# Kernel optimization log

Measured on AMD Instinct MI355X. Metric: run time of the kernel, lower is better.

## Reference

```python
import jax, jax.numpy as jnp
import numpy as np

B, S, E, FFN, Q = 8, 2048, 512, 2048, 8


def setup_inputs() -> dict:
    key = jax.random.key(0)
    k0, k1, k2, k3 = jax.random.split(key, 4)
    x = jax.random.normal(k0, (B, S, E), dtype=jnp.float32)
    ry = jax.random.normal(k1, (Q,), dtype=jnp.float32)  # trainable RY angles
    w1 = jax.random.normal(k2, (FFN, Q), dtype=jnp.float32) / np.sqrt(Q).astype(np.float32)
    b1 = jnp.zeros((FFN,), dtype=jnp.float32)
    w2 = jax.random.normal(k3, (E, FFN), dtype=jnp.float32) / np.sqrt(FFN).astype(np.float32)
    b2 = jnp.zeros((E,), dtype=jnp.float32)
    return {"x": x, "ry": ry, "w1": w1, "b1": b1, "w2": w2, "b2": b2}


def reference(x, ry, w1, b1, w2, b2):
    # Quantum layer: each qubit i starts in |0>, gets RX(x[..., i]) then RY(ry[i]),
    # then PauliZ expectation. Product state => closed form <Z_i> = cos(x_i) * cos(ry_i).
    nq = ry.shape[0]
    z = jnp.cos(x[..., :nq]) * jnp.cos(ry)  # [B, S, Q]
    # dropout is identity in eval mode
    h = jnp.einsum("bsq,fq->bsf", z, w1) + b1  # fc1
    return jnp.einsum("bsf,ef->bse", jax.nn.relu(h), w2) + b2  # fc2
```

## Files before the change

### kernel.cpp

```cpp
#include <hip/hip_runtime.h>
#include <cstdint>
#include <cstddef>


typedef __attribute__((ext_vector_type(8))) short s16x8;
typedef __attribute__((ext_vector_type(4))) float f32x4;

__device__ __forceinline__ unsigned short f2bf(float f) {
  unsigned int u = __float_as_uint(f);
  unsigned int r = u + 0x7fffu + ((u >> 16) & 1u);
  return (unsigned short)(r >> 16);
}

__device__ __forceinline__ void async_copy16(const void* g, void* l) {
  __builtin_amdgcn_global_load_lds(
      (const __attribute__((address_space(1))) void*)(uintptr_t)g,
      (__attribute__((address_space(3))) void*)(unsigned int)(uintptr_t)l,
      16, 0, 0);
}

__global__ __launch_bounds__(256) void k_w2(const float* __restrict__ w2,
                                            unsigned short* __restrict__ img) {
  const int n = blockIdx.x;
  const int t = threadIdx.x;
  const int s = t >> 2, quad = t & 3;
  const float* src = w2 + (size_t)n * 2048 + t * 8;
  float4 a = *(const float4*)src;
  float4 b = *(const float4*)(src + 4);
  uint4 pk;
  pk.x = f2bf(a.x) | ((unsigned)f2bf(a.y) << 16);
  pk.y = f2bf(a.z) | ((unsigned)f2bf(a.w) << 16);
  pk.z = f2bf(b.x) | ((unsigned)f2bf(b.y) << 16);
  pk.w = f2bf(b.z) | ((unsigned)f2bf(b.w) << 16);
  const int nt = n >> 8, nl = n & 255, nhi = nl >> 4, nlo = nl & 15;
  const size_t ci = (size_t)(nt * 64 + s) * 1024 + nhi * 64 + quad * 16 + nlo;
  *(uint4*)(img + ci * 8) = pk;
}

__global__ __launch_bounds__(256, 2) void k_fused(
    const float* __restrict__ x, const float* __restrict__ ry,
    const float* __restrict__ w1, const float* __restrict__ b1,
    const unsigned short* __restrict__ w2b, const float* __restrict__ b2,
    float* __restrict__ C) {
  __shared__ unsigned short As[2][64 * 32];
  __shared__ unsigned short Bs[2][256 * 32];
  __shared__ float b1s[2048];

  const int t = threadIdx.x;
  const int lane = t & 63;
  const int w = t >> 6;
  const int mt = (int)(blockIdx.x >> 1);
  const int nt = (int)(blockIdx.x & 1);
  const int r0 = mt * 64;
  const int c0 = nt * 256;
  const int fp = t & 15;
  const int rq = t >> 4;

  float zr[4][8];
  {
    float4 ra = *(const float4*)ry;
    float4 rb = *(const float4*)(ry + 4);
    float cy[8] = {__cosf(ra.x), __cosf(ra.y), __cosf(ra.z), __cosf(ra.w),
                   __cosf(rb.x), __cosf(rb.y), __cosf(rb.z), __cosf(rb.w)};
#pragma unroll
    for (int r = 0; r < 4; ++r) {
      const float* xr = x + (size_t)(r0 + rq * 4 + r) * 512;
      float4 x0 = *(const float4*)xr;
      float4 x1 = *(const float4*)(xr + 4);
      zr[r][0] = __cosf(x0.x) * cy[0];
      zr[r][1] = __cosf(x0.y) * cy[1];
      zr[r][2] = __cosf(x0.z) * cy[2];
      zr[r][3] = __cosf(x0.w) * cy[3];
      zr[r][4] = __cosf(x1.x) * cy[4];
      zr[r][5] = __cosf(x1.y) * cy[5];
      zr[r][6] = __cosf(x1.z) * cy[6];
      zr[r][7] = __cosf(x1.w) * cy[7];
    }
  }
  __builtin_amdgcn_sched_barrier(0);

  f32x4 wA0, wA1, wA2, wA3, wB0, wB1, wB2, wB3;
  {
    const f32x4* p0 = (const f32x4*)(w1 + fp * 16);
    wA0 = p0[0]; wA1 = p0[1]; wA2 = p0[2]; wA3 = p0[3];
    const f32x4* p1 = (const f32x4*)(w1 + 256 + fp * 16);
    wB0 = p1[0]; wB1 = p1[1]; wB2 = p1[2]; wB3 = p1[3];
  }
  __builtin_amdgcn_sched_barrier(0);

  const unsigned short* gB = w2b + (size_t)nt * 524288 + t * 8;
  char* lB = (char*)Bs + t * 16;
  auto stage = [&](int s, int buf) {
#pragma unroll
    for (int p = 0; p < 4; ++p)
      async_copy16(gB + (size_t)s * 8192 + p * 2048,
                   lB + buf * 16384 + p * 4096);
  };
  stage(0, 0);
  async_copy16(b1 + (size_t)t * 4, (char*)b1s + (size_t)t * 16);
  async_copy16(b1 + (size_t)(t + 256) * 4, (char*)b1s + (size_t)(t + 256) * 16);
  stage(1, 1);

  asm volatile("s_waitcnt vmcnt(4) lgkmcnt(0)" ::: "memory");
  __builtin_amdgcn_sched_barrier(0);
  __builtin_amdgcn_s_barrier();

  char* aswr = (char*)As + (rq >> 2) * 1024 +
               (((((fp >> 3) & 1) << 3) | ((rq & 3) << 1) | ((fp >> 2) & 1)) << 4) +
               (fp & 3) * 4;
  auto act = [&](int s, int buf, const f32x4& v0, const f32x4& v1,
                 const f32x4& v2, const f32x4& v3) {
    float b0 = b1s[s * 32 + fp * 2];
    float b1v = b1s[s * 32 + fp * 2 + 1];
    char* dst = aswr + buf * 4096;
#pragma unroll
    for (int r = 0; r < 4; ++r) {
      float h0 = b0, h1 = b1v;
      h0 += zr[r][0] * v0[0]; h1 += zr[r][0] * v2[0];
      h0 += zr[r][1] * v0[1]; h1 += zr[r][1] * v2[1];
      h0 += zr[r][2] * v0[2]; h1 += zr[r][2] * v2[2];
      h0 += zr[r][3] * v0[3]; h1 += zr[r][3] * v2[3];
      h0 += zr[r][4] * v1[0]; h1 += zr[r][4] * v3[0];
      h0 += zr[r][5] * v1[1]; h1 += zr[r][5] * v3[1];
      h0 += zr[r][6] * v1[2]; h1 += zr[r][6] * v3[2];
      h0 += zr[r][7] * v1[3]; h1 += zr[r][7] * v3[3];
      h0 = fmaxf(h0, 0.0f);
      h1 = fmaxf(h1, 0.0f);
      unsigned int u;
      asm("v_cvt_pk_bf16_f32 %0, %1, %2" : "=v"(u) : "v"(h0), "v"(h1));
      *(unsigned int*)(dst + r * 256) = u;
    }
  };

  act(0, 0, wA0, wA1, wA2, wA3);

  const int wn = w * 64;
  const int fr = lane & 15;
  const int quad = lane >> 4;
  const int slotA = ((fr & 3) << 4) | (((quad >> 1) & 1) << 3) |
                    ((fr >> 2) << 1) | (quad & 1);
  const char* pAb = (const char*)As + slotA * 16;
  const char* pBb = (const char*)Bs + w * 4096 + quad * 256 + fr * 16;

  f32x4 acc[4][4];
#pragma unroll
  for (int i = 0; i < 4; ++i)
#pragma unroll
    for (int j = 0; j < 4; ++j) acc[i][j] = (f32x4){0.f, 0.f, 0.f, 0.f};

  auto body = [&](int kt, const f32x4& u0, const f32x4& u1, const f32x4& u2,
                  const f32x4& u3, f32x4& l0, f32x4& l1, f32x4& l2,
                  f32x4& l3) {
    asm volatile("s_waitcnt vmcnt(4) lgkmcnt(0)" ::: "memory");
    __builtin_amdgcn_sched_barrier(0);
    __builtin_amdgcn_s_barrier();

    {
      const f32x4* p = (const f32x4*)(w1 + (size_t)(kt + 2) * 256 + fp * 16);
      l0 = p[0]; l1 = p[1]; l2 = p[2]; l3 = p[3];
    }
    const int cur = kt & 1;
    s16x8 af[4], bfv[4];
    const char* pA = pAb + cur * 4096;
    const char* pB = pBb + cur * 16384;
#pragma unroll
    for (int i = 0; i < 4; ++i) af[i] = *(const s16x8*)(pA + i * 1024);
#pragma unroll
    for (int j = 0; j < 4; ++j) bfv[j] = *(const s16x8*)(pB + j * 1024);

    act(kt + 1, cur ^ 1, u0, u1, u2, u3);

    __builtin_amdgcn_s_setprio(1);
#pragma unroll
    for (int i = 0; i < 4; ++i)
#pragma unroll
      for (int j = 0; j < 4; ++j)
        acc[i][j] = __builtin_amdgcn_mfma_f32_16x16x32_bf16(af[i], bfv[j],
                                                            acc[i][j], 0, 0, 0);
    __builtin_amdgcn_s_setprio(0);

    asm volatile("s_waitcnt lgkmcnt(0)" ::: "memory");
    __builtin_amdgcn_sched_barrier(0);
    __builtin_amdgcn_s_barrier();

    stage(kt + 2, cur);
  };

  for (int kt = 0; kt < 62; kt += 2) {
    body(kt, wB0, wB1, wB2, wB3, wA0, wA1, wA2, wA3);
    body(kt + 1, wA0, wA1, wA2, wA3, wB0, wB1, wB2, wB3);
  }

  {
    asm volatile("s_waitcnt vmcnt(4) lgkmcnt(0)" ::: "memory");
    __builtin_amdgcn_sched_barrier(0);
    __builtin_amdgcn_s_barrier();
    s16x8 af[4], bfv[4];
#pragma unroll
    for (int i = 0; i < 4; ++i) af[i] = *(const s16x8*)(pAb + i * 1024);
#pragma unroll
    for (int j = 0; j < 4; ++j) bfv[j] = *(const s16x8*)(pBb + j * 1024);
    act(63, 1, wB0, wB1, wB2, wB3);
    __builtin_amdgcn_s_setprio(1);
#pragma unroll
    for (int i = 0; i < 4; ++i)
#pragma unroll
      for (int j = 0; j < 4; ++j)
        acc[i][j] = __builtin_amdgcn_mfma_f32_16x16x32_bf16(af[i], bfv[j],
                                                            acc[i][j], 0, 0, 0);
    __builtin_amdgcn_s_setprio(0);
    asm volatile("s_waitcnt lgkmcnt(0)" ::: "memory");
    __builtin_amdgcn_sched_barrier(0);
    __builtin_amdgcn_s_barrier();
  }
  {
    asm volatile("s_waitcnt vmcnt(0) lgkmcnt(0)" ::: "memory");
    __builtin_amdgcn_sched_barrier(0);
    __builtin_amdgcn_s_barrier();
    s16x8 af[4], bfv[4];
#pragma unroll
    for (int i = 0; i < 4; ++i)
      af[i] = *(const s16x8*)(pAb + 4096 + i * 1024);
#pragma unroll
    for (int j = 0; j < 4; ++j)
      bfv[j] = *(const s16x8*)(pBb + 16384 + j * 1024);
#pragma unroll
    for (int i = 0; i < 4; ++i)
#pragma unroll
      for (int j = 0; j < 4; ++j)
        acc[i][j] = __builtin_amdgcn_mfma_f32_16x16x32_bf16(af[i], bfv[j],
                                                            acc[i][j], 0, 0, 0);
  }

  float bias[4];
#pragma unroll
  for (int j = 0; j < 4; ++j) bias[j] = b2[c0 + wn + j * 16 + fr];
#pragma unroll
  for (int i = 0; i < 4; ++i) {
    const int rbase = r0 + i * 16 + quad * 4;
#pragma unroll
    for (int rr = 0; rr < 4; ++rr) {
      float* crow = C + (size_t)(rbase + rr) * 512;
#pragma unroll
      for (int j = 0; j < 4; ++j)
        crow[c0 + wn + j * 16 + fr] = acc[i][j][rr] + bias[j];
    }
  }
}

__global__ __launch_bounds__(256) void k_naive(
    const float* __restrict__ x, const float* __restrict__ ry,
    const float* __restrict__ w1, const float* __restrict__ b1,
    const float* __restrict__ w2, const float* __restrict__ b2,
    float* __restrict__ out) {
  __shared__ float zsh[8];
  __shared__ float acts[2048];
  const int r = blockIdx.x;
  const int t = threadIdx.x;
  if (t < 8) zsh[t] = __cosf(x[(size_t)r * 512 + t]) * __cosf(ry[t]);
  __syncthreads();
  float z[8];
#pragma unroll
  for (int q = 0; q < 8; ++q) z[q] = zsh[q];
#pragma unroll
  for (int i = 0; i < 8; ++i) {
    const int f = t * 8 + i;
    const float* wr = w1 + (size_t)f * 8;
    float4 a = *(const float4*)wr;
    float4 b = *(const float4*)(wr + 4);
    float h = b1[f] + z[0] * a.x + z[1] * a.y + z[2] * a.z + z[3] * a.w +
              z[4] * b.x + z[5] * b.y + z[6] * b.z + z[7] * b.w;
    acts[f] = fmaxf(h, 0.0f);
  }
  __syncthreads();
  for (int ee = 0; ee < 2; ++ee) {
    const int e = t + ee * 256;
    const float* wr = w2 + (size_t)e * 2048;
    float acc = b2[e];
    for (int f = 0; f < 2048; f += 4) {
      float4 wv = *(const float4*)(wr + f);
      float4 av = *(const float4*)(acts + f);
      acc += av.x * wv.x + av.y * wv.y + av.z * wv.z + av.w * wv.w;
    }
    out[(size_t)r * 512 + e] = acc;
  }
}

extern "C" void kernel_launch(void* const* d_in, const int* in_sizes, int n_in,
                              void* d_out, int out_size, void* d_ws,
                              size_t ws_size, hipStream_t stream) {
  const float* x  = (const float*)d_in[0];
  const float* ry = (const float*)d_in[1];
  const float* w1 = (const float*)d_in[2];
  const float* b1 = (const float*)d_in[3];
  const float* w2 = (const float*)d_in[4];
  const float* b2 = (const float*)d_in[5];
  float* out = (float*)d_out;

  const size_t w2b_bytes = (size_t)512 * 2048 * 2;
  if (ws_size < w2b_bytes) {
    k_naive<<<dim3(16384), dim3(256), 0, stream>>>(x, ry, w1, b1, w2, b2, out);
    return;
  }
  unsigned short* w2b = (unsigned short*)d_ws;
  k_w2<<<dim3(512), dim3(256), 0, stream>>>(w2, w2b);
  k_fused<<<dim3(512), dim3(256), 0, stream>>>(x, ry, w1, b1, w2b, b2, out);
}
```

Before: 149.9 us.

## Triple-buffer W2 tiles, drop second barrier, and XOR-swizzle activation LDS layout

Expands the B shared-memory staging from double to triple buffering, so the next tile's async load can be issued right after the first barrier of each step and the trailing barrier per k-step can be removed. The A-tile activation layout in LDS is changed to an XOR-swizzled row layout, with the writes reorganised to cut bank conflicts on stores and fragment reads. The main loop is unrolled by six with explicit buffer rotation. The extra LDS buffer raises shared-memory use per block, which may limit occupancy, and the waitcnt accounting is tricky to get right.

After: 150.7 us. No clear change (+0.5%).

```diff
diff --git a/kernel.cpp b/kernel.cpp
--- a/kernel.cpp
+++ b/kernel.cpp
@@ -43,7 +43,7 @@
     const unsigned short* __restrict__ w2b, const float* __restrict__ b2,
     float* __restrict__ C) {
   __shared__ unsigned short As[2][64 * 32];
-  __shared__ unsigned short Bs[2][256 * 32];
+  __shared__ unsigned short Bs[3][256 * 32];
   __shared__ float b1s[2048];
 
   const int t = threadIdx.x;
@@ -79,6 +79,20 @@
   }
   __builtin_amdgcn_sched_barrier(0);
 
+  const unsigned short* gB = w2b + (size_t)nt * 524288 + t * 8;
+  char* lB = (char*)Bs + t * 16;
+  auto stage = [&](int s, int buf) {
+#pragma unroll
+    for (int p = 0; p < 4; ++p)
+      async_copy16(gB + (size_t)s * 8192 + p * 2048,
+                   lB + buf * 16384 + p * 4096);
+  };
+  async_copy16(b1 + (size_t)t * 4, (char*)b1s + (size_t)t * 16);
+  async_copy16(b1 + (size_t)(t + 256) * 4, (char*)b1s + (size_t)(t + 256) * 16);
+  stage(0, 0);
+  stage(1, 1);
+  __builtin_amdgcn_sched_barrier(0);
+
   f32x4 wA0, wA1, wA2, wA3, wB0, wB1, wB2, wB3;
   {
     const f32x4* p0 = (const f32x4*)(w1 + fp * 16);
@@ -86,50 +100,47 @@
     const f32x4* p1 = (const f32x4*)(w1 + 256 + fp * 16);
     wB0 = p1[0]; wB1 = p1[1]; wB2 = p1[2]; wB3 = p1[3];
   }
-  __builtin_amdgcn_sched_barrier(0);
-
-  const unsigned short* gB = w2b + (size_t)nt * 524288 + t * 8;
-  char* lB = (char*)Bs + t * 16;
-  auto stage = [&](int s, int buf) {
-#pragma unroll
-    for (int p = 0; p < 4; ++p)
-      async_copy16(gB + (size_t)s * 8192 + p * 2048,
-                   lB + buf * 16384 + p * 4096);
-  };
-  stage(0, 0);
-  async_copy16(b1 + (size_t)t * 4, (char*)b1s + (size_t)t * 16);
-  async_copy16(b1 + (size_t)(t + 256) * 4, (char*)b1s + (size_t)(t + 256) * 16);
-  stage(1, 1);
-
-  asm volatile("s_waitcnt vmcnt(4) lgkmcnt(0)" ::: "memory");
+
+  asm volatile("s_waitcnt vmcnt(12) lgkmcnt(0)" ::: "memory");
   __builtin_amdgcn_sched_barrier(0);
   __builtin_amdgcn_s_barrier();
 
-  char* aswr = (char*)As + (rq >> 2) * 1024 +
-               (((((fp >> 3) & 1) << 3) | ((rq & 3) << 1) | ((fp >> 2) & 1)) << 4) +
-               (fp & 3) * 4;
+  const int q0 = rq & 1;
+  const int koct = fp >> 2, fpl = fp & 3;
+  const int sA_off = ((koct ^ ((rq * 2) & 3)) << 4) + fpl * 4;
+  const int sB_off = ((koct ^ ((rq * 2 + 1) & 3)) << 4) + fpl * 4;
+  const int rw0 = ((rq * 4 + 0) ^ q0) * 64;
+  const int rw1 = ((rq * 4 + 1) ^ q0) * 64;
+  const int rw2 = ((rq * 4 + 2) ^ q0) * 64;
+  const int rw3 = ((rq * 4 + 3) ^ q0) * 64;
+
   auto act = [&](int s, int buf, const f32x4& v0, const f32x4& v1,
                  const f32x4& v2, const f32x4& v3) {
-    float b0 = b1s[s * 32 + fp * 2];
-    float b1v = b1s[s * 32 + fp * 2 + 1];
-    char* dst = aswr + buf * 4096;
-#pragma unroll
-    for (int r = 0; r < 4; ++r) {
-      float h0 = b0, h1 = b1v;
-      h0 += zr[r][0] * v0[0]; h1 += zr[r][0] * v2[0];
-      h0 += zr[r][1] * v0[1]; h1 += zr[r][1] * v2[1];
-      h0 += zr[r][2] * v0[2]; h1 += zr[r][2] * v2[2];
-      h0 += zr[r][3] * v0[3]; h1 += zr[r][3] * v2[3];
-      h0 += zr[r][4] * v1[0]; h1 += zr[r][4] * v3[0];
-      h0 += zr[r][5] * v1[1]; h1 += zr[r][5] * v3[1];
-      h0 += zr[r][6] * v1[2]; h1 += zr[r][6] * v3[2];
-      h0 += zr[r][7] * v1[3]; h1 += zr[r][7] * v3[3];
-      h0 = fmaxf(h0, 0.0f);
-      h1 = fmaxf(h1, 0.0f);
-      unsigned int u;
-      asm("v_cvt_pk_bf16_f32 %0, %1, %2" : "=v"(u) : "v"(h0), "v"(h1));
-      *(unsigned int*)(dst + r * 256) = u;
-    }
+    const float bb0 = b1s[s * 32 + fp * 2];
+    const float bb1 = b1s[s * 32 + fp * 2 + 1];
+    unsigned int u0, u1, u2, u3;
+#define ACT_ROW(R, UD)                                                      \
+  {                                                                         \
+    float h0 = bb0, h1 = bb1;                                               \
+    h0 += zr[R][0] * v0[0]; h1 += zr[R][0] * v2[0];                         \
+    h0 += zr[R][1] * v0[1]; h1 += zr[R][1] * v2[1];                         \
+    h0 += zr[R][2] * v0[2]; h1 += zr[R][2] * v2[2];                         \
+    h0 += zr[R][3] * v0[3]; h1 += zr[R][3] * v2[3];                         \
+    h0 += zr[R][4] * v1[0]; h1 += zr[R][4] * v3[0];                         \
+    h0 += zr[R][5] * v1[1]; h1 += zr[R][5] * v3[1];                         \
+    h0 += zr[R][6] * v1[2]; h1 += zr[R][6] * v3[2];                         \
+    h0 += zr[R][7] * v1[3]; h1 += zr[R][7] * v3[3];                         \
+    h0 = fmaxf(h0, 0.0f);                                                   \
+    h1 = fmaxf(h1, 0.0f);                                                   \
+    asm("v_cvt_pk_bf16_f32 %0, %1, %2" : "=v"(UD) : "v"(h0), "v"(h1));      \
+  }
+    ACT_ROW(0, u0) ACT_ROW(1, u1) ACT_ROW(2, u2) ACT_ROW(3, u3)
+#undef ACT_ROW
+    char* base = (char*)As + buf * 4096;
+    *(unsigned int*)(base + rw0 + sA_off) = q0 ? u1 : u0;
+    *(unsigned int*)(base + rw1 + sA_off) = q0 ? u0 : u1;
+    *(unsigned int*)(base + rw2 + sB_off) = q0 ? u3 : u2;
+    *(unsigned int*)(base + rw3 + sB_off) = q0 ? u2 : u3;
   };
 
   act(0, 0, wA0, wA1, wA2, wA3);
@@ -137,9 +148,8 @@
   const int wn = w * 64;
   const int fr = lane & 15;
   const int quad = lane >> 4;
-  const int slotA = ((fr & 3) << 4) | (((quad >> 1) & 1) << 3) |
-                    ((fr >> 2) << 1) | (quad & 1);
-  const char* pAb = (const char*)As + slotA * 16;
+  const char* pAb =
+      (const char*)As + fr * 64 + ((quad ^ ((fr >> 1) & 3)) << 4);
   const char* pBb = (const char*)Bs + w * 4096 + quad * 256 + fr * 16;
 
   f32x4 acc[4][4];
@@ -148,89 +158,52 @@
 #pragma unroll
     for (int j = 0; j < 4; ++j) acc[i][j] = (f32x4){0.f, 0.f, 0.f, 0.f};
 
-  auto body = [&](int kt, const f32x4& u0, const f32x4& u1, const f32x4& u2,
-                  const f32x4& u3, f32x4& l0, f32x4& l1, f32x4& l2,
-                  f32x4& l3) {
-    asm volatile("s_waitcnt vmcnt(4) lgkmcnt(0)" ::: "memory");
-    __builtin_amdgcn_sched_barrier(0);
-    __builtin_amdgcn_s_barrier();
-
-    {
-      const f32x4* p = (const f32x4*)(w1 + (size_t)(kt + 2) * 256 + fp * 16);
-      l0 = p[0]; l1 = p[1]; l2 = p[2]; l3 = p[3];
-    }
-    const int cur = kt & 1;
-    s16x8 af[4], bfv[4];
-    const char* pA = pAb + cur * 4096;
-    const char* pB = pBb + cur * 16384;
-#pragma unroll
-    for (int i = 0; i < 4; ++i) af[i] = *(const s16x8*)(pA + i * 1024);
-#pragma unroll
-    for (int j = 0; j < 4; ++j) bfv[j] = *(const s16x8*)(pB + j * 1024);
-
-    act(kt + 1, cur ^ 1, u0, u1, u2, u3);
-
-    __builtin_amdgcn_s_setprio(1);
-#pragma unroll
-    for (int i = 0; i < 4; ++i)
-#pragma unroll
-      for (int j = 0; j < 4; ++j)
-        acc[i][j] = __builtin_amdgcn_mfma_f32_16x16x32_bf16(af[i], bfv[j],
-                                                            acc[i][j], 0, 0, 0);
-    __builtin_amdgcn_s_setprio(0);
-
-    asm volatile("s_waitcnt lgkmcnt(0)" ::: "memory");
-    __builtin_amdgcn_sched_barrier(0);
-    __builtin_amdgcn_s_barrier();
-
-    stage(kt + 2, cur);
-  };
-
-  for (int kt = 0; kt < 62; kt += 2) {
-    body(kt, wB0, wB1, wB2, wB3, wA0, wA1, wA2, wA3);
-    body(kt + 1, wA0, wA1, wA2, wA3, wB0, wB1, wB2, wB3);
-  }
-
-  {
-    asm volatile("s_waitcnt vmcnt(4) lgkmcnt(0)" ::: "memory");
-    __builtin_amdgcn_sched_barrier(0);
-    __builtin_amdgcn_s_barrier();
-    s16x8 af[4], bfv[4];
-#pragma unroll
-    for (int i = 0; i < 4; ++i) af[i] = *(const s16x8*)(pAb + i * 1024);
-#pragma unroll
-    for (int j = 0; j < 4; ++j) bfv[j] = *(const s16x8*)(pBb + j * 1024);
-    act(63, 1, wB0, wB1, wB2, wB3);
-    __builtin_amdgcn_s_setprio(1);
-#pragma unroll
-    for (int i = 0; i < 4; ++i)
-#pragma unroll
-      for (int j = 0; j < 4; ++j)
-        acc[i][j] = __builtin_amdgcn_mfma_f32_16x16x32_bf16(af[i], bfv[j],
-                                                            acc[i][j], 0, 0, 0);
-    __builtin_amdgcn_s_setprio(0);
-    asm volatile("s_waitcnt lgkmcnt(0)" ::: "memory");
-    __builtin_amdgcn_sched_barrier(0);
-    __builtin_amdgcn_s_barrier();
-  }
-  {
-    asm volatile("s_waitcnt vmcnt(0) lgkmcnt(0)" ::: "memory");
-    __builtin_amdgcn_sched_barrier(0);
-    __builtin_amdgcn_s_barrier();
-    s16x8 af[4], bfv[4];
-#pragma unroll
-    for (int i = 0; i < 4; ++i)
-      af[i] = *(const s16x8*)(pAb + 4096 + i * 1024);
-#pragma unroll
-    for (int j = 0; j < 4; ++j)
-      bfv[j] = *(const s16x8*)(pBb + 16384 + j * 1024);
-#pragma unroll
-    for (int i = 0; i < 4; ++i)
-#pragma unroll
-      for (int j = 0; j < 4; ++j)
-        acc[i][j] = __builtin_amdgcn_mfma_f32_16x16x32_bf16(af[i], bfv[j],
-                                                            acc[i][j], 0, 0, 0);
-  }
+#define BODY(KT, BUF, BUF2, L0, L1, L2, L3, U0, U1, U2, U3, PRE, ACTG, VMC) \
+  {                                                                         \
+    asm volatile("s_waitcnt vmcnt(" VMC ") lgkmcnt(0)" ::: "memory");       \
+    __builtin_amdgcn_sched_barrier(0);                                      \
+    __builtin_amdgcn_s_barrier();                                           \
+    if (PRE) {                                                              \
+      stage((KT) + 2, BUF2);                                                \
+      const f32x4* wp =                                                     \
+          (const f32x4*)(w1 + (size_t)((KT) + 2) * 256 + fp * 16);          \
+      L0 = wp[0]; L1 = wp[1]; L2 = wp[2]; L3 = wp[3];                       \
+    }                                                                       \
+    s16x8 af[4], bfv[4];                                                    \
+    {                                                                       \
+      const char* pA = pAb + ((KT) & 1) * 4096;                             \
+      const char* pB = pBb + (BUF) * 16384;                                 \
+      af[0] = *(const s16x8*)(pA);                                          \
+      af[1] = *(const s16x8*)(pA + 1024);                                   \
+      af[2] = *(const s16x8*)(pA + 2048);                                   \
+      af[3] = *(const s16x8*)(pA + 3072);                                   \
+      bfv[0] = *(const s16x8*)(pB);                                         \
+      bfv[1] = *(const s16x8*)(pB + 1024);                                  \
+      bfv[2] = *(const s16x8*)(pB + 2048);                                  \
+      bfv[3] = *(const s16x8*)(pB + 3072);                                  \
+    }                                                                       \
+    if (ACTG) act((KT) + 1, ((KT) + 1) & 1, U0, U1, U2, U3);                \
+    __builtin_amdgcn_s_setprio(1);                                          \
+    _Pragma("unroll") for (int i = 0; i < 4; ++i)                           \
+        _Pragma("unroll") for (int j = 0; j < 4; ++j) acc[i][j] =           \
+        __builtin_amdgcn_mfma_f32_16x16x32_bf16(af[i], bfv[j], acc[i][j],   \
+                                                0, 0, 0);                   \
+    __builtin_amdgcn_s_setprio(0);                                          \
+  }
+
+  for (int kt = 0; kt < 60; kt += 6) {
+    BODY(kt + 0, 0, 2, wA0, wA1, wA2, wA3, wB0, wB1, wB2, wB3, true, true, "8");
+    BODY(kt + 1, 1, 0, wB0, wB1, wB2, wB3, wA0, wA1, wA2, wA3, true, true, "8");
+    BODY(kt + 2, 2, 1, wA0, wA1, wA2, wA3, wB0, wB1, wB2, wB3, true, true, "8");
+    BODY(kt + 3, 0, 2, wB0, wB1, wB2, wB3, wA0, wA1, wA2, wA3, true, true, "8");
+    BODY(kt + 4, 1, 0, wA0, wA1, wA2, wA3, wB0, wB1, wB2, wB3, true, true, "8");
+    BODY(kt + 5, 2, 1, wB0, wB1, wB2, wB3, wA0, wA1, wA2, wA3, true, true, "8");
+  }
+  BODY(60, 0, 2, wA0, wA1, wA2, wA3, wB0, wB1, wB2, wB3, true, true, "8");
+  BODY(61, 1, 0, wB0, wB1, wB2, wB3, wA0, wA1, wA2, wA3, true, true, "8");
+  BODY(62, 2, 1, wA0, wA1, wA2, wA3, wB0, wB1, wB2, wB3, false, true, "8");
+  BODY(63, 0, 2, wB0, wB1, wB2, wB3, wA0, wA1, wA2, wA3, false, false, "4");
+#undef BODY
 
   float bias[4];
 #pragma unroll
```
